# Optimization experiments

Measured on AMD Instinct MI355X. Metric: run time of the kernel, lower is better.

## Reference

```python
import jax, jax.numpy as jnp
import numpy as np

D_IN = 1024
D_OUT = 1024
NUM_HEADS = 16
DIM_HEAD = D_OUT // NUM_HEADS


def setup_inputs() -> dict:
    key = jax.random.key(0)
    ks = jax.random.split(key, 6)
    s = 0.02
    x = jax.random.normal(ks[0], (2, 2048, D_IN), dtype=jnp.float32)
    Wk = jax.random.normal(ks[1], (D_IN, D_OUT), dtype=jnp.float32) * s
    Wq = jax.random.normal(ks[2], (D_IN, D_OUT), dtype=jnp.float32) * s
    Wv = jax.random.normal(ks[3], (D_IN, D_OUT), dtype=jnp.float32) * s
    Wo = jax.random.normal(ks[4], (D_OUT, D_OUT), dtype=jnp.float32) * s
    bo = jax.random.normal(ks[5], (D_OUT,), dtype=jnp.float32) * s
    return {"x": x, "Wk": Wk, "Wq": Wq, "Wv": Wv, "Wo": Wo, "bo": bo}


def reference(x, Wk, Wq, Wv, Wo, bo):
    B, S, _ = x.shape
    # projections -> [B, H, S, Dh]
    def split_heads(t):
        return t.reshape(B, S, NUM_HEADS, DIM_HEAD).transpose(0, 2, 1, 3)
    q = split_heads(x @ Wq)
    k = split_heads(x @ Wk)
    v = split_heads(x @ Wv)
    # NOTE: source uses non-in-place masked_fill whose result is discarded,
    # so NO causal mask is actually applied (faithful reproduction).
    scores = jnp.einsum("bhqd,bhkd->bhqk", q, k) / jnp.sqrt(jnp.float32(DIM_HEAD))
    wgts = jax.nn.softmax(scores, axis=-1)  # dropout = identity (eval mode)
    ctx = jnp.einsum("bhqk,bhkd->bhqd", wgts, v)
    ctx = ctx.transpose(0, 2, 1, 3).reshape(B, S, D_OUT)
    return ctx @ Wo + bo
```

## Files before the change

kernel.cpp:

```cpp
#include <hip/hip_runtime.h>
#include <stdint.h>

typedef short bf16x8 __attribute__((ext_vector_type(8)));
typedef float f32x4  __attribute__((ext_vector_type(4)));
typedef unsigned int u32x4 __attribute__((ext_vector_type(4)));
typedef unsigned int u32x2 __attribute__((ext_vector_type(2)));

__device__ __forceinline__ unsigned short f2bf(float f) {
  unsigned int u = __builtin_bit_cast(unsigned int, f) + 0x8000u;
  return (unsigned short)(u >> 16);
}
__device__ __forceinline__ unsigned int pack2bf(float a, float b) {
  unsigned int ua = __builtin_bit_cast(unsigned int, a) + 0x8000u;
  unsigned int ub = __builtin_bit_cast(unsigned int, b) + 0x8000u;
  return __builtin_amdgcn_perm(ub, ua, 0x07060302);
}

__device__ __forceinline__ void gl2lds16(const void* g, void* l) {
  __builtin_amdgcn_global_load_lds(
      (const __attribute__((address_space(1))) void*)g,
      (__attribute__((address_space(3))) void*)l, 16, 0, 0);
}

template <int N> __device__ __forceinline__ void wait_vmcnt() {
  asm volatile("s_waitcnt vmcnt(%0)" ::"n"(N) : "memory");
}

__global__ __launch_bounds__(256) void cast_x_k(const float* __restrict__ x,
                                                unsigned short* __restrict__ xb) {
  int i = blockIdx.x * 256 + threadIdx.x;
  float4 v = ((const float4*)x)[i];
  u32x2 o;
  o.x = pack2bf(v.x, v.y);
  o.y = pack2bf(v.z, v.w);
  ((u32x2*)xb)[i] = o;
}

__global__ __launch_bounds__(256) void castT_k(
    const float* __restrict__ Wq, const float* __restrict__ Wk,
    const float* __restrict__ Wv, const float* __restrict__ Wo,
    unsigned short* __restrict__ Tq, unsigned short* __restrict__ Tk,
    unsigned short* __restrict__ Tv, unsigned short* __restrict__ To) {
  __shared__ float tile[32][33];
  const int z = blockIdx.z;
  const float* W = (z == 0) ? Wq : (z == 1) ? Wk : (z == 2) ? Wv : Wo;
  unsigned short* T = (z == 0) ? Tq : (z == 1) ? Tk : (z == 2) ? Tv : To;
  const int tx = threadIdx.x, ty = threadIdx.y;
  const int n0 = blockIdx.x * 32, k0 = blockIdx.y * 32;
#pragma unroll
  for (int j = 0; j < 32; j += 8)
    tile[ty + j][tx] = W[(size_t)(k0 + ty + j) * 1024 + n0 + tx];
  __syncthreads();
#pragma unroll
  for (int j = 0; j < 32; j += 8)
    T[(size_t)(n0 + ty + j) * 1024 + k0 + tx] = f2bf(tile[tx][ty + j]);
}

template <int MODE, int TN>
__global__ __launch_bounds__(256) void gemm_bt_k(const unsigned short* __restrict__ A,
                                                 const unsigned short* __restrict__ B,
                                                 void* __restrict__ C,
                                                 const float* __restrict__ bias,
                                                 int K) {
  __shared__ alignas(16) short lA[3][512 * 8];
  __shared__ alignas(16) short lB[3][128 * TN * 8];
  constexpr int PT = 2 + TN / 2;
  const int tid = threadIdx.x;
  const int wid = tid >> 6, lane = tid & 63;
  const int l15 = lane & 15, quad = lane >> 4;
  const int waveM = wid >> 1, waveN = wid & 1;
  const int bm = blockIdx.y * 128, bn = blockIdx.x * (32 * TN);

  f32x4 acc[4][TN];
#pragma unroll
  for (int i = 0; i < 4; ++i)
#pragma unroll
    for (int j = 0; j < TN; ++j) acc[i][j] = (f32x4){0.f, 0.f, 0.f, 0.f};

  auto stage = [&](int kk, short* la, short* lb) {
#pragma unroll
    for (int j = 0; j < 2; ++j) {
      int c = tid + 256 * j;
      int row = ((c >> 6) << 4) | (c & 15);
      int ch = (c >> 4) & 3;
      gl2lds16(A + (size_t)(bm + row) * K + kk + ch * 8, &la[(c & ~63) * 8]);
    }
#pragma unroll
    for (int j = 0; j < TN / 2; ++j) {
      int c = tid + 256 * j;
      int row = ((c >> 6) << 4) | (c & 15);
      int ch = (c >> 4) & 3;
      gl2lds16(B + (size_t)(bn + row) * K + kk + ch * 8, &lb[(c & ~63) * 8]);
    }
  };

  auto compute = [&](const short* la, const short* lb) {
    bf16x8 af[4], bfr[TN];
#pragma unroll
    for (int i = 0; i < 4; ++i)
      af[i] = *(const bf16x8*)&la[(((waveM * 4 + i) * 64) + lane) * 8];
#pragma unroll
    for (int j = 0; j < TN; ++j)
      bfr[j] = *(const bf16x8*)&lb[(((waveN * TN + j) * 64) + lane) * 8];
#pragma unroll
    for (int i = 0; i < 4; ++i)
#pragma unroll
      for (int j = 0; j < TN; ++j)
        acc[i][j] = __builtin_amdgcn_mfma_f32_16x16x32_bf16(af[i], bfr[j], acc[i][j], 0, 0, 0);
  };

  const int NT = K >> 5;
  short *pa0 = lA[0], *pa1 = lA[1], *pa2 = lA[2];
  short *pb0 = lB[0], *pb1 = lB[1], *pb2 = lB[2];
  stage(0, pa0, pb0);
  stage(32, pa1, pb1);
#pragma unroll 1
  for (int t = 0; t < NT - 1; ++t) {
    wait_vmcnt<PT>();
    __builtin_amdgcn_sched_barrier(0);
    __builtin_amdgcn_s_barrier();
    __builtin_amdgcn_sched_barrier(0);
    if (t + 2 < NT) stage((t + 2) * 32, pa2, pb2);
    compute(pa0, pb0);
    short* ta = pa0; pa0 = pa1; pa1 = pa2; pa2 = ta;
    short* tb = pb0; pb0 = pb1; pb1 = pb2; pb2 = tb;
  }
  wait_vmcnt<0>();
  __builtin_amdgcn_sched_barrier(0);
  __builtin_amdgcn_s_barrier();
  __builtin_amdgcn_sched_barrier(0);
  compute(pa0, pb0);

#pragma unroll
  for (int i = 0; i < 4; ++i)
#pragma unroll
    for (int j = 0; j < TN; ++j) {
      int row = bm + waveM * 64 + i * 16 + quad * 4;
      int col = bn + (waveN * TN + j) * 16 + l15;
      if (MODE == 0) {
        unsigned short* Cq = (unsigned short*)C;
        int w = col >> 10, n1 = col & 1023;
        int h = n1 >> 6, d = n1 & 63;
        int b = row >> 11, s = row & 2047;
        int bhh = (b << 4) + h;
        if (w == 2) {
          int g = (i << 2) + quad;
          int ks2 = g >> 3, rem = g & 7;
          int pos = ((ks2 << 2) + (rem & 3)) * 8 + (rem >> 2) * 4;
          u32x2 pk;
          pk.x = pack2bf(acc[i][j][0], acc[i][j][1]);
          pk.y = pack2bf(acc[i][j][2], acc[i][j][3]);
          *(u32x2*)&Cq[(size_t)2 * 4194304 + ((size_t)bhh * 64 + d) * 2048 +
                       (s & ~63) + pos] = pk;
        } else {
          float sc = (w == 0) ? 0.18033688011112042f : 1.0f;
#pragma unroll
          for (int r = 0; r < 4; ++r)
            Cq[(size_t)w * 4194304 + ((size_t)bhh * 2048 + s + r) * 64 + d] =
                f2bf(acc[i][j][r] * sc);
        }
      } else {
#pragma unroll
        for (int r = 0; r < 4; ++r)
          ((float*)C)[(size_t)(row + r) * 1024 + col] = acc[i][j][r] + bias[col];
      }
    }
}

__global__ __launch_bounds__(128) void flash_k(const unsigned short* __restrict__ Qh,
                                               const unsigned short* __restrict__ Kh,
                                               const unsigned short* __restrict__ Vt,
                                               unsigned short* __restrict__ ctxb) {
  constexpr int SL = 2048;
  __shared__ alignas(16) short kt[2][512 * 8];
  __shared__ alignas(16) short vt[2][512 * 8];

  const int tid = threadIdx.x;
  const int wid = tid >> 6, lane = tid & 63;
  const int l15 = lane & 15, quad = lane >> 4;
  const int bh = blockIdx.y;
  const int q0 = blockIdx.x * 64 + wid * 32;

  const unsigned short* Qb = Qh + (size_t)bh * SL * 64;
  const unsigned short* Kb = Kh + (size_t)bh * SL * 64;
  const unsigned short* Vb = Vt + (size_t)bh * 64 * SL;

  bf16x8 qf[2][2];
#pragma unroll
  for (int s = 0; s < 2; ++s)
#pragma unroll
    for (int ks = 0; ks < 2; ++ks)
      qf[s][ks] = *(const bf16x8*)(Qb + (size_t)(q0 + s * 16 + l15) * 64 + ks * 32 + quad * 8);

  f32x4 o[2][4];
  f32x4 rs4[2] = {(f32x4){0.f, 0.f, 0.f, 0.f}, (f32x4){0.f, 0.f, 0.f, 0.f}};
  const f32x4 z4 = (f32x4){0.f, 0.f, 0.f, 0.f};
#pragma unroll
  for (int s = 0; s < 2; ++s)
#pragma unroll
    for (int t = 0; t < 4; ++t) o[s][t] = z4;

  auto stage = [&](int kb, short* ktb, short* vtb) {
#pragma unroll
    for (int j2 = 0; j2 < 4; ++j2) {
      int cc = tid + 128 * j2;
      int row = cc >> 3;
      int ko = (cc & 7) ^ (row & 7);
      gl2lds16(Kb + (size_t)(kb + row) * 64 + ko * 8, &ktb[(cc & ~63) * 8]);
      gl2lds16(Vb + (size_t)row * SL + kb + ko * 8, &vtb[(cc & ~63) * 8]);
    }
  };

  auto compute = [&](const short* ktb, const short* vtb) {
    f32x4 sv[2][4];
#pragma unroll
    for (int t = 0; t < 4; ++t) {
      int key = t * 16 + l15;
      bf16x8 kf0 = *(bf16x8*)&ktb[(key * 8 + (quad ^ (key & 7))) * 8];
      bf16x8 kf1 = *(bf16x8*)&ktb[(key * 8 + ((4 + quad) ^ (key & 7))) * 8];
#pragma unroll
      for (int s = 0; s < 2; ++s) {
        sv[s][t] = __builtin_amdgcn_mfma_f32_16x16x32_bf16(kf0, qf[s][0], z4, 0, 0, 0);
        sv[s][t] = __builtin_amdgcn_mfma_f32_16x16x32_bf16(kf1, qf[s][1], sv[s][t], 0, 0, 0);
      }
    }
    u32x4 pf[2][2];
#pragma unroll
    for (int s = 0; s < 2; ++s)
#pragma unroll
      for (int t = 0; t < 4; ++t) {
        f32x4 p;
#pragma unroll
        for (int r = 0; r < 4; ++r) p[r] = __builtin_amdgcn_exp2f(sv[s][t][r]);
        rs4[s] += p;
        pf[s][t >> 1][(t & 1) * 2 + 0] = pack2bf(p[0], p[1]);
        pf[s][t >> 1][(t & 1) * 2 + 1] = pack2bf(p[2], p[3]);
      }
#pragma unroll
    for (int t = 0; t < 4; ++t) {
      int d = t * 16 + l15;
#pragma unroll
      for (int ks = 0; ks < 2; ++ks) {
        bf16x8 vf = *(bf16x8*)&vtb[(d * 8 + ((ks * 4 + quad) ^ (d & 7))) * 8];
#pragma unroll
        for (int s = 0; s < 2; ++s)
          o[s][t] = __builtin_amdgcn_mfma_f32_16x16x32_bf16(
              vf, __builtin_bit_cast(bf16x8, pf[s][ks]), o[s][t], 0, 0, 0);
      }
    }
  };

  stage(0, kt[0], vt[0]);
#pragma unroll 1
  for (int i2 = 0; i2 < 16; ++i2) {
    __syncthreads();
    stage((2 * i2 + 1) * 64, kt[1], vt[1]);
    compute(kt[0], vt[0]);
    __syncthreads();
    if (i2 < 15) stage((2 * i2 + 2) * 64, kt[0], vt[0]);
    compute(kt[1], vt[1]);
  }

  const int bb = bh >> 4, h = bh & 15;
#pragma unroll
  for (int s = 0; s < 2; ++s) {
    float v = (rs4[s][0] + rs4[s][1]) + (rs4[s][2] + rs4[s][3]);
    v += __shfl_xor(v, 16);
    v += __shfl_xor(v, 32);
    float inv = 1.0f / v;
    int tok = q0 + s * 16 + l15;
    size_t base = ((size_t)(bb * 2048 + tok)) * 1024 + h * 64;
#pragma unroll
    for (int t = 0; t < 4; ++t) {
      u32x2 pk;
      pk.x = pack2bf(o[s][t][0] * inv, o[s][t][1] * inv);
      pk.y = pack2bf(o[s][t][2] * inv, o[s][t][3] * inv);
      *(u32x2*)&ctxb[base + t * 16 + quad * 4] = pk;
    }
  }
}

extern "C" void kernel_launch(void* const* d_in, const int* in_sizes, int n_in,
                              void* d_out, int out_size, void* d_ws, size_t ws_size,
                              hipStream_t stream) {
  const float* x  = (const float*)d_in[0];
  const float* Wk = (const float*)d_in[1];
  const float* Wq = (const float*)d_in[2];
  const float* Wv = (const float*)d_in[3];
  const float* Wo = (const float*)d_in[4];
  const float* bo = (const float*)d_in[5];
  float* out = (float*)d_out;

  char* ws = (char*)d_ws;
  const size_t MB = 1u << 20;
  unsigned short* xb   = (unsigned short*)(ws);
  unsigned short* WqT  = (unsigned short*)(ws + 8  * MB);
  unsigned short* WkT  = (unsigned short*)(ws + 10 * MB);
  unsigned short* WvT  = (unsigned short*)(ws + 12 * MB);
  unsigned short* WoT  = (unsigned short*)(ws + 14 * MB);
  unsigned short* Qh   = (unsigned short*)(ws + 16 * MB);
  unsigned short* ctxb = xb;

  cast_x_k<<<4096, 256, 0, stream>>>(x, xb);
  castT_k<<<dim3(32, 32, 4), dim3(32, 8), 0, stream>>>(Wq, Wk, Wv, Wo, WqT, WkT, WvT, WoT);
  gemm_bt_k<0, 4><<<dim3(24, 32), 256, 0, stream>>>(xb, WqT, Qh, nullptr, 1024);
  flash_k<<<dim3(32, 32), 128, 0, stream>>>(Qh, Qh + 4194304, Qh + 2 * 4194304, ctxb);
  gemm_bt_k<1, 2><<<dim3(16, 32), 256, 0, stream>>>(ctxb, WoT, out, bo, 1024);
}
```

Baseline: 221.0 us.

## Triple-buffer flash attention K/V staging with 256-thread blocks and head-grouped grid

```diff
diff --git a/kernel.cpp b/kernel.cpp
--- a/kernel.cpp
+++ b/kernel.cpp
@@ -167,19 +167,21 @@
     }
 }
 
-__global__ __launch_bounds__(128) void flash_k(const unsigned short* __restrict__ Qh,
+__global__ __launch_bounds__(256) void flash_k(const unsigned short* __restrict__ Qh,
                                                const unsigned short* __restrict__ Kh,
                                                const unsigned short* __restrict__ Vt,
                                                unsigned short* __restrict__ ctxb) {
   constexpr int SL = 2048;
-  __shared__ alignas(16) short kt[2][512 * 8];
-  __shared__ alignas(16) short vt[2][512 * 8];
+  __shared__ alignas(16) short kt[3][512 * 8];
+  __shared__ alignas(16) short vt[3][512 * 8];
 
   const int tid = threadIdx.x;
   const int wid = tid >> 6, lane = tid & 63;
   const int l15 = lane & 15, quad = lane >> 4;
-  const int bh = blockIdx.y;
-  const int q0 = blockIdx.x * 64 + wid * 32;
+  const int bid = blockIdx.x;
+  const int jj = bid >> 3;
+  const int bh = ((bid & 7) << 2) | (jj >> 4);
+  const int q0 = (jj & 15) * 128 + wid * 32;
 
   const unsigned short* Qb = Qh + (size_t)bh * SL * 64;
   const unsigned short* Kb = Kh + (size_t)bh * SL * 64;
@@ -202,8 +204,8 @@
 
   auto stage = [&](int kb, short* ktb, short* vtb) {
 #pragma unroll
-    for (int j2 = 0; j2 < 4; ++j2) {
-      int cc = tid + 128 * j2;
+    for (int j2 = 0; j2 < 2; ++j2) {
+      int cc = tid + 256 * j2;
       int row = cc >> 3;
       int ko = (cc & 7) ^ (row & 7);
       gl2lds16(Kb + (size_t)(kb + row) * 64 + ko * 8, &ktb[(cc & ~63) * 8]);
@@ -250,16 +252,26 @@
     }
   };
 
-  stage(0, kt[0], vt[0]);
+  short *k0 = kt[0], *k1 = kt[1], *k2 = kt[2];
+  short *v0 = vt[0], *v1 = vt[1], *v2 = vt[2];
+  stage(0, k0, v0);
+  stage(64, k1, v1);
 #pragma unroll 1
-  for (int i2 = 0; i2 < 16; ++i2) {
-    __syncthreads();
-    stage((2 * i2 + 1) * 64, kt[1], vt[1]);
-    compute(kt[0], vt[0]);
-    __syncthreads();
-    if (i2 < 15) stage((2 * i2 + 2) * 64, kt[0], vt[0]);
-    compute(kt[1], vt[1]);
+  for (int t = 0; t < 31; ++t) {
+    wait_vmcnt<4>();
+    __builtin_amdgcn_sched_barrier(0);
+    __builtin_amdgcn_s_barrier();
+    __builtin_amdgcn_sched_barrier(0);
+    if (t + 2 < 32) stage((t + 2) * 64, k2, v2);
+    compute(k0, v0);
+    short* tk = k0; k0 = k1; k1 = k2; k2 = tk;
+    short* tv = v0; v0 = v1; v1 = v2; v2 = tv;
   }
+  wait_vmcnt<0>();
+  __builtin_amdgcn_sched_barrier(0);
+  __builtin_amdgcn_s_barrier();
+  __builtin_amdgcn_sched_barrier(0);
+  compute(k0, v0);
 
   const int bb = bh >> 4, h = bh & 15;
 #pragma unroll
@@ -304,6 +316,6 @@
   cast_x_k<<<4096, 256, 0, stream>>>(x, xb);
   castT_k<<<dim3(32, 32, 4), dim3(32, 8), 0, stream>>>(Wq, Wk, Wv, Wo, WqT, WkT, WvT, WoT);
   gemm_bt_k<0, 4><<<dim3(24, 32), 256, 0, stream>>>(xb, WqT, Qh, nullptr, 1024);
-  flash_k<<<dim3(32, 32), 128, 0, stream>>>(Qh, Qh + 4194304, Qh + 2 * 4194304, ctxb);
+  flash_k<<<512, 256, 0, stream>>>(Qh, Qh + 4194304, Qh + 2 * 4194304, ctxb);
   gemm_bt_k<1, 2><<<dim3(16, 32), 256, 0, stream>>>(ctxb, WoT, out, bo, 1024);
 }
```

After: 211.7 us. 4.2% less time.
